# Optimization experiments

Hardware: AMD Instinct MI355X
Metric: run time of the kernel (lower is better)

Reference implementation:

```python
import jax, jax.numpy as jnp
import numpy as np

N = 100000
E = 1600000
D_IN = 50
D_H = 128
D_OUT = 128
EPS = 1e-5


def setup_inputs() -> dict:
    key = jax.random.key(0)
    ks = jax.random.split(key, 24)
    def w(k, shape, fan_in):
        return jax.random.normal(k, shape, jnp.float32) / np.sqrt(fan_in)
    inp = {
        'x': jax.random.normal(ks[0], (N, D_IN), jnp.float32),
        'edge_src': jax.random.randint(ks[1], (E,), 0, N, jnp.int32),
        'edge_dst': jax.random.randint(ks[2], (E,), 0, N, jnp.int32),
        # SAGEConv 1: D_IN -> D_H
        'Wl1': w(ks[3], (D_IN, D_H), D_IN), 'Wr1': w(ks[4], (D_IN, D_H), D_IN), 'b1': jnp.zeros((D_H,), jnp.float32),
        # SAGEConv 2: D_H -> D_H
        'Wl2': w(ks[5], (D_H, D_H), D_H), 'Wr2': w(ks[6], (D_H, D_H), D_H), 'b2': jnp.zeros((D_H,), jnp.float32),
        # SAGEConv 3: D_H -> D_OUT
        'Wl3': w(ks[7], (D_H, D_OUT), D_H), 'Wr3': w(ks[8], (D_H, D_OUT), D_H), 'b3': jnp.zeros((D_OUT,), jnp.float32),
        # skip linears (no bias)
        'Ws1': w(ks[9], (D_IN, D_H), D_IN), 'Ws2': w(ks[10], (D_IN, D_H), D_IN),
        # LayerNorm affine
        'lnw1': jnp.ones((D_H,), jnp.float32), 'lnb1': jnp.zeros((D_H,), jnp.float32),
        'lnw2': jnp.ones((D_H,), jnp.float32), 'lnb2': jnp.zeros((D_H,), jnp.float32),
        'lnw3': jnp.ones((D_OUT,), jnp.float32), 'lnb3': jnp.zeros((D_OUT,), jnp.float32),
        # PReLU scalar slopes (PyG init 0.25)
        'a1': jnp.float32(0.25), 'a2': jnp.float32(0.25), 'a3': jnp.float32(0.25),
    }
    return inp


def _sage(x, src, dst, Wl, Wr, b):
    # mean aggregation of source features at destinations, then linear + root
    msg = x[src]                                              # [E, d]
    agg = jax.ops.segment_sum(msg, dst, num_segments=N)       # [N, d]
    cnt = jax.ops.segment_sum(jnp.ones((src.shape[0],), x.dtype), dst, num_segments=N)
    mean = agg / jnp.maximum(cnt, 1.0)[:, None]
    return mean @ Wl + x @ Wr + b


def _graph_ln(x, w, b):
    # PyG LayerNorm mode='graph', batch=None: normalize over all nodes+channels
    xc = x - jnp.mean(x)
    std = jnp.sqrt(jnp.mean(xc * xc))
    return (xc / (std + EPS)) * w + b


def _prelu(x, a):
    return jnp.where(x >= 0, x, a * x)


def reference(x, edge_src, edge_dst, Wl1, Wr1, b1, Wl2, Wr2, b2, Wl3, Wr3, b3,
              Ws1, Ws2, lnw1, lnb1, lnw2, lnb2, lnw3, lnb3, a1, a2, a3):
    h1 = _sage(x, edge_src, edge_dst, Wl1, Wr1, b1)
    h1 = _prelu(_graph_ln(h1, lnw1, lnb1), a1)
    h2 = _sage(h1 + x @ Ws1, edge_src, edge_dst, Wl2, Wr2, b2)
    h2 = _prelu(_graph_ln(h2, lnw2, lnb2), a2)
    ret = _sage(h1 + h2 + x @ Ws2, edge_src, edge_dst, Wl3, Wr3, b3)
    ret = _prelu(_graph_ln(ret, lnw3, lnb3), a3)
    return ret
```

## Files before the change

kernel.cpp:

```cpp
#include <hip/hip_runtime.h>

#define D_IN 50
#define LN_EPS 1e-5f
#define BSH 8
#define MAXB 512

typedef __bf16 bf16_t;
typedef bf16_t bf16x8 __attribute__((ext_vector_type(8)));
typedef bf16_t bf16x4 __attribute__((ext_vector_type(4)));
typedef bf16_t bf16x2 __attribute__((ext_vector_type(2)));
typedef float f32x4_t __attribute__((ext_vector_type(4)));
typedef float f32x2_t __attribute__((ext_vector_type(2)));

#define ACCP(r, A)                                                            \
    {                                                                         \
        A[0] += (f32x2_t){__uint_as_float((r).x << 16),                       \
                          __uint_as_float((r).x & 0xffff0000u)};              \
        A[1] += (f32x2_t){__uint_as_float((r).y << 16),                       \
                          __uint_as_float((r).y & 0xffff0000u)};              \
        A[2] += (f32x2_t){__uint_as_float((r).z << 16),                       \
                          __uint_as_float((r).z & 0xffff0000u)};              \
        A[3] += (f32x2_t){__uint_as_float((r).w << 16),                       \
                          __uint_as_float((r).w & 0xffff0000u)};              \
    }

__global__ void bucket_hist_k(const int* __restrict__ dst, int* __restrict__ bcnt,
                              int e, int nb) {
    __shared__ int lh[MAXB];
    int t = threadIdx.x;
    for (int i = t; i < nb; i += 256) lh[i] = 0;
    __syncthreads();
    for (int i = blockIdx.x * 256 + t; i < e; i += gridDim.x * 256)
        atomicAdd(&lh[dst[i] >> BSH], 1);
    __syncthreads();
    for (int i = t; i < nb; i += 256) {
        int c = lh[i];
        if (c) atomicAdd(&bcnt[i * 16], c);
    }
}

__global__ void bscan_k(const int* __restrict__ bcnt, int* __restrict__ boff,
                        int* __restrict__ bpos, int nb, int e) {
    __shared__ int l[MAXB];
    int t = threadIdx.x;
    l[t] = (t < nb) ? bcnt[t * 16] : 0;
    __syncthreads();
    for (int off = 1; off < MAXB; off <<= 1) {
        int v = (t >= off) ? l[t - off] : 0;
        __syncthreads();
        l[t] += v;
        __syncthreads();
    }
    int excl = (t > 0) ? l[t - 1] : 0;
    if (t < nb) { boff[t] = excl; bpos[t * 16] = excl; }
    if (t == 0) boff[nb] = e;
}

__global__ void scatter_k(const int* __restrict__ src, const int* __restrict__ dst,
                          int* __restrict__ bpos, unsigned* __restrict__ pool,
                          int e, int nb) {
    __shared__ int lh[MAXB];
    __shared__ int lcur[MAXB];
    int t = threadIdx.x;
    for (int i = t; i < nb; i += 256) lh[i] = 0;
    __syncthreads();
    int chunk = (e + gridDim.x - 1) / gridDim.x;
    int s = blockIdx.x * chunk;
    int en = min(e, s + chunk);
    for (int i = s + t; i < en; i += 256)
        atomicAdd(&lh[dst[i] >> BSH], 1);
    __syncthreads();
    for (int i = t; i < nb; i += 256) {
        int c = lh[i];
        lcur[i] = c ? atomicAdd(&bpos[i * 16], c) : 0;
    }
    __syncthreads();
    for (int i = s + t; i < en; i += 256) {
        int d = dst[i];
        int p = atomicAdd(&lcur[d >> BSH], 1);
        pool[p] = (unsigned)src[i] | ((unsigned)(d & 255) << 17);
    }
}

__global__ void nhist_cfill_k(const unsigned* __restrict__ pool, const int* __restrict__ boff,
                              int* __restrict__ rp, int* __restrict__ col, int n) {
    __shared__ int lc[256];
    __shared__ int ls[256];
    __shared__ int lpos[256];
    int b = blockIdx.x, t = threadIdx.x;
    lc[t] = 0;
    __syncthreads();
    int s = boff[b], e = boff[b + 1];
    for (int i = s + t; i < e; i += 256) atomicAdd(&lc[pool[i] >> 17], 1);
    __syncthreads();
    int v = lc[t];
    ls[t] = v;
    __syncthreads();
    for (int off = 1; off < 256; off <<= 1) {
        int x = (t >= off) ? ls[t - off] : 0;
        __syncthreads();
        ls[t] += x;
        __syncthreads();
    }
    int excl = ls[t] - v;
    int nd = (b << BSH) + t;
    if (nd < n) rp[nd] = s + excl;
    if (nd == n - 1) rp[n] = e;
    lpos[t] = s + excl;
    __syncthreads();
    for (int i = s + t; i < e; i += 256) {
        unsigned pk = pool[i];
        int slot = atomicAdd(&lpos[pk >> 17], 1);
        col[slot] = (int)(pk & 0x1FFFFu);
    }
}

struct ConvDesc { const float* w; bf16_t* o; int kin; int kpad; };
struct ConvArgs { ConvDesc d[8]; };

__global__ void conv_w_k(ConvArgs args) {
    ConvDesc d = args.d[blockIdx.y];
    int i = blockIdx.x * 256 + threadIdx.x;
    int tot = 128 * d.kpad;
    if (i >= tot) return;
    int n = i / d.kpad, k = i - n * d.kpad;
    float v = (k < d.kin) ? d.w[(size_t)k * 128 + n] : 0.f;
    d.o[i] = (bf16_t)v;
}

__global__ void conv_x_k(const float* __restrict__ x, bf16_t* __restrict__ xb, int n) {
    int i = blockIdx.x * 256 + threadIdx.x;
    if (i >= n * 64) return;
    int node = i >> 6, k = i & 63;
    xb[i] = (k < D_IN) ? (bf16_t)x[node * D_IN + k] : (bf16_t)0.f;
}

__global__ void agg_bf64_k(const bf16_t* __restrict__ feat, const int* __restrict__ rp,
                           const int* __restrict__ col, bf16_t* __restrict__ mean, int n) {
    int wid = (blockIdx.x * blockDim.x + threadIdx.x) >> 6;
    int lane = threadIdx.x & 63;
    if (wid >= n) return;
    int start = rp[wid], end = rp[wid + 1];
    int lc = lane & 7;
    int g = lane >> 3;
    f32x2_t accA[4], accB[4];
#pragma unroll
    for (int k = 0; k < 4; k++) { accA[k] = (f32x2_t){0.f, 0.f}; accB[k] = (f32x2_t){0.f, 0.f}; }
    int e = start + g;
    if (e + 8 < end) {
        int i0 = col[e], i1 = col[e + 8];
        for (; e + 24 < end; e += 16) {
            uint4 r0 = *(const uint4*)(feat + (size_t)i0 * 64 + lc * 8);
            uint4 r1 = *(const uint4*)(feat + (size_t)i1 * 64 + lc * 8);
            i0 = col[e + 16];
            i1 = col[e + 24];
            ACCP(r0, accA);
            ACCP(r1, accB);
        }
        uint4 r0 = *(const uint4*)(feat + (size_t)i0 * 64 + lc * 8);
        uint4 r1 = *(const uint4*)(feat + (size_t)i1 * 64 + lc * 8);
        ACCP(r0, accA);
        ACCP(r1, accB);
        e += 16;
    }
    for (; e < end; e += 8) {
        uint4 r0 = *(const uint4*)(feat + (size_t)col[e] * 64 + lc * 8);
        ACCP(r0, accA);
    }
#pragma unroll
    for (int k = 0; k < 4; k++) accA[k] += accB[k];
    float aL[4], aH[4];
#pragma unroll
    for (int k = 0; k < 4; k++) { aL[k] = accA[k].x; aH[k] = accA[k].y; }
#pragma unroll
    for (int off = 8; off < 64; off <<= 1) {
#pragma unroll
        for (int k = 0; k < 4; k++) {
            aL[k] += __shfl_xor(aL[k], off);
            aH[k] += __shfl_xor(aH[k], off);
        }
    }
    int c = end - start;
    float invc = 1.f / (float)(c > 0 ? c : 1);
    if (lane < 8) {
        bf16x8 o;
#pragma unroll
        for (int k = 0; k < 4; k++) {
            o[2 * k] = (bf16_t)(aL[k] * invc);
            o[2 * k + 1] = (bf16_t)(aH[k] * invc);
        }
        *(bf16x8*)(mean + (size_t)wid * 64 + lc * 8) = o;
    }
}

__global__ void agg_bf128_k(const bf16_t* __restrict__ feat, const int* __restrict__ rp,
                            const int* __restrict__ col, bf16_t* __restrict__ mean, int n) {
    int wid = (blockIdx.x * blockDim.x + threadIdx.x) >> 6;
    int lane = threadIdx.x & 63;
    if (wid >= n) return;
    int start = rp[wid], end = rp[wid + 1];
    int lc = lane & 15;
    int g = lane >> 4;
    const uint* fp = (const uint*)feat + lc * 4;
    f32x2_t accA[4], accB[4];
#pragma unroll
    for (int k = 0; k < 4; k++) { accA[k] = (f32x2_t){0.f, 0.f}; accB[k] = (f32x2_t){0.f, 0.f}; }
    int e = start + g;
    int ng = (e < end) ? (((end - 1 - e) >> 2) + 1) : 0;
    int it = 0;
    for (; it + 4 <= ng; it += 4, e += 16) {
        int a = col[e], b = col[e + 4], c = col[e + 8], d = col[e + 12];
        uint4 r0 = *(const uint4*)(fp + (size_t)a * 64);
        uint4 r1 = *(const uint4*)(fp + (size_t)b * 64);
        uint4 r2 = *(const uint4*)(fp + (size_t)c * 64);
        uint4 r3 = *(const uint4*)(fp + (size_t)d * 64);
        ACCP(r0, accA);
        ACCP(r1, accB);
        ACCP(r2, accA);
        ACCP(r3, accB);
    }
    int rem = ng - it;
    if (rem > 0) {
        int a = col[e];
        int b = (rem > 1) ? col[e + 4] : a;
        int c = (rem > 2) ? col[e + 8] : b;
        uint4 r0 = *(const uint4*)(fp + (size_t)a * 64);
        uint4 r1 = *(const uint4*)(fp + (size_t)b * 64);
        uint4 r2 = *(const uint4*)(fp + (size_t)c * 64);
        ACCP(r0, accA);
        if (rem > 1) ACCP(r1, accB);
        if (rem > 2) ACCP(r2, accA);
    }
#pragma unroll
    for (int k = 0; k < 4; k++) accA[k] += accB[k];
    float aL[4], aH[4];
#pragma unroll
    for (int k = 0; k < 4; k++) { aL[k] = accA[k].x; aH[k] = accA[k].y; }
#pragma unroll
    for (int off = 16; off < 64; off <<= 1) {
#pragma unroll
        for (int k = 0; k < 4; k++) {
            aL[k] += __shfl_xor(aL[k], off);
            aH[k] += __shfl_xor(aH[k], off);
        }
    }
    int c = end - start;
    float invc = 1.f / (float)(c > 0 ? c : 1);
    if (lane < 16) {
        bf16x8 o;
#pragma unroll
        for (int k = 0; k < 4; k++) {
            o[2 * k] = (bf16_t)(aL[k] * invc);
            o[2 * k + 1] = (bf16_t)(aH[k] * invc);
        }
        *(bf16x8*)(mean + (size_t)wid * 128 + lc * 8) = o;
    }
}

template <int KPAD, bool DUAL, bool ACC>
__global__ __launch_bounds__(256) void mfma_gemm_k(
    const bf16_t* __restrict__ A, const bf16_t* __restrict__ B,
    const bf16_t* __restrict__ WlT, const bf16_t* __restrict__ WrT,
    const float* __restrict__ bias,
    bf16_t* __restrict__ out, float2* __restrict__ partials, int M) {
    constexpr int KC = KPAD / 32;
    constexpr int WELE = 8 * KC * 64 * 8;
    __shared__ bf16_t lwl[WELE];
    __shared__ bf16_t lwr[DUAL ? WELE : 8];

    const int tid = threadIdx.x;
    for (int ch = tid; ch < 8 * KC * 64; ch += 256) {
        int nt = ch / (KC * 64);
        int rem = ch - nt * (KC * 64);
        int c = rem >> 6;
        int ln = rem & 63;
        int m = ln & 15, q = ln >> 4;
        size_t srcoff = (size_t)(nt * 16 + m) * KPAD + c * 32 + q * 8;
        *(bf16x8*)&lwl[ch * 8] = *(const bf16x8*)(WlT + srcoff);
        if (DUAL) *(bf16x8*)&lwr[ch * 8] = *(const bf16x8*)(WrT + srcoff);
    }
    __syncthreads();

    const int wid = blockIdx.x * 4 + (tid >> 6);
    const int lane = tid & 63;
    const int row0 = wid * 32;
    if (row0 >= M) return;
    const int m = lane & 15;
    const int q = lane >> 4;

    bf16x8 af[2][KC], bfr[DUAL ? 2 : 1][DUAL ? KC : 1];
#pragma unroll
    for (int s = 0; s < 2; s++) {
        const bf16_t* ar = A + (size_t)(row0 + s * 16 + m) * KPAD + q * 8;
#pragma unroll
        for (int c = 0; c < KC; c++) af[s][c] = *(const bf16x8*)(ar + c * 32);
        if (DUAL) {
            const bf16_t* br = B + (size_t)(row0 + s * 16 + m) * KPAD + q * 8;
#pragma unroll
            for (int c = 0; c < KC; c++) bfr[s][c] = *(const bf16x8*)(br + c * 32);
        }
    }

    float lsum = 0.f, lsum2 = 0.f;
#pragma unroll
    for (int nt = 0; nt < 8; nt++) {
        f32x4_t acc0 = {0.f, 0.f, 0.f, 0.f};
        f32x4_t acc1 = {0.f, 0.f, 0.f, 0.f};
#pragma unroll
        for (int c = 0; c < KC; c++) {
            bf16x8 w = *(const bf16x8*)&lwl[((nt * KC + c) * 64 + lane) * 8];
            acc0 = __builtin_amdgcn_mfma_f32_16x16x32_bf16(af[0][c], w, acc0, 0, 0, 0);
            acc1 = __builtin_amdgcn_mfma_f32_16x16x32_bf16(af[1][c], w, acc1, 0, 0, 0);
        }
        if (DUAL) {
#pragma unroll
            for (int c = 0; c < KC; c++) {
                bf16x8 w = *(const bf16x8*)&lwr[((nt * KC + c) * 64 + lane) * 8];
                acc0 = __builtin_amdgcn_mfma_f32_16x16x32_bf16(bfr[0][c], w, acc0, 0, 0, 0);
                acc1 = __builtin_amdgcn_mfma_f32_16x16x32_bf16(bfr[1][c], w, acc1, 0, 0, 0);
            }
        }
        float bv = bias ? bias[nt * 16 + m] : 0.f;
#pragma unroll
        for (int s = 0; s < 2; s++) {
            f32x4_t* ap = (s == 0) ? &acc0 : &acc1;
#pragma unroll
            for (int r = 0; r < 4; r++) {
                int row = row0 + s * 16 + q * 4 + r;
                if (row < M) {
                    float o = (*ap)[r] + bv;
                    out[(size_t)row * 128 + nt * 16 + m] = (bf16_t)o;
                    if (ACC) { lsum += o; lsum2 += o * o; }
                }
            }
        }
    }
    if (ACC) {
        for (int off = 32; off > 0; off >>= 1) {
            lsum += __shfl_down(lsum, off);
            lsum2 += __shfl_down(lsum2, off);
        }
        if (lane == 0) partials[wid] = make_float2(lsum, lsum2);
    }
}

__global__ __launch_bounds__(256) void mfma_gemm3_k(
    const bf16_t* __restrict__ A, const bf16_t* __restrict__ B,
    const bf16_t* __restrict__ WlT, const bf16_t* __restrict__ WrT,
    const bf16_t* __restrict__ Ws1T, const bf16_t* __restrict__ Ws2T,
    const float* __restrict__ bias,
    bf16_t* __restrict__ outP, bf16_t* __restrict__ outC1, bf16_t* __restrict__ outC2,
    float2* __restrict__ partials, int M) {
    constexpr int KC = 2;
    constexpr int WELE = 8 * KC * 64 * 8;
    __shared__ bf16_t lwl[WELE];
    __shared__ bf16_t lwr[WELE];
    __shared__ bf16_t ls1[WELE];
    __shared__ bf16_t ls2[WELE];

    const int tid = threadIdx.x;
    for (int ch = tid; ch < 8 * KC * 64; ch += 256) {
        int nt = ch / (KC * 64);
        int rem = ch - nt * (KC * 64);
        int c = rem >> 6;
        int ln = rem & 63;
        int m = ln & 15, q = ln >> 4;
        size_t srcoff = (size_t)(nt * 16 + m) * 64 + c * 32 + q * 8;
        *(bf16x8*)&lwl[ch * 8] = *(const bf16x8*)(WlT + srcoff);
        *(bf16x8*)&lwr[ch * 8] = *(const bf16x8*)(WrT + srcoff);
        *(bf16x8*)&ls1[ch * 8] = *(const bf16x8*)(Ws1T + srcoff);
        *(bf16x8*)&ls2[ch * 8] = *(const bf16x8*)(Ws2T + srcoff);
    }
    __syncthreads();

    const int wid = blockIdx.x * 4 + (tid >> 6);
    const int lane = tid & 63;
    const int row0 = wid * 32;
    if (row0 >= M) return;
    const int m = lane & 15;
    const int q = lane >> 4;

    bf16x8 af[2][KC], bfr[2][KC];
#pragma unroll
    for (int s = 0; s < 2; s++) {
        const bf16_t* ar = A + (size_t)(row0 + s * 16 + m) * 64 + q * 8;
        const bf16_t* br = B + (size_t)(row0 + s * 16 + m) * 64 + q * 8;
#pragma unroll
        for (int c = 0; c < KC; c++) {
            af[s][c] = *(const bf16x8*)(ar + c * 32);
            bfr[s][c] = *(const bf16x8*)(br + c * 32);
        }
    }

    float lsum = 0.f, lsum2 = 0.f;
#pragma unroll
    for (int nt = 0; nt < 8; nt++) {
        f32x4_t aP0 = {0.f, 0.f, 0.f, 0.f}, aP1 = {0.f, 0.f, 0.f, 0.f};
        f32x4_t a10 = {0.f, 0.f, 0.f, 0.f}, a11 = {0.f, 0.f, 0.f, 0.f};
        f32x4_t a20 = {0.f, 0.f, 0.f, 0.f}, a21 = {0.f, 0.f, 0.f, 0.f};
#pragma unroll
        for (int c = 0; c < KC; c++) {
            int wi = ((nt * KC + c) * 64 + lane) * 8;
            bf16x8 wl = *(const bf16x8*)&lwl[wi];
            bf16x8 wr = *(const bf16x8*)&lwr[wi];
            bf16x8 w1 = *(const bf16x8*)&ls1[wi];
            bf16x8 w2 = *(const bf16x8*)&ls2[wi];
            aP0 = __builtin_amdgcn_mfma_f32_16x16x32_bf16(af[0][c], wl, aP0, 0, 0, 0);
            aP1 = __builtin_amdgcn_mfma_f32_16x16x32_bf16(af[1][c], wl, aP1, 0, 0, 0);
            aP0 = __builtin_amdgcn_mfma_f32_16x16x32_bf16(bfr[0][c], wr, aP0, 0, 0, 0);
            aP1 = __builtin_amdgcn_mfma_f32_16x16x32_bf16(bfr[1][c], wr, aP1, 0, 0, 0);
            a10 = __builtin_amdgcn_mfma_f32_16x16x32_bf16(bfr[0][c], w1, a10, 0, 0, 0);
            a11 = __builtin_amdgcn_mfma_f32_16x16x32_bf16(bfr[1][c], w1, a11, 0, 0, 0);
            a20 = __builtin_amdgcn_mfma_f32_16x16x32_bf16(bfr[0][c], w2, a20, 0, 0, 0);
            a21 = __builtin_amdgcn_mfma_f32_16x16x32_bf16(bfr[1][c], w2, a21, 0, 0, 0);
        }
        float bv = bias[nt * 16 + m];
#pragma unroll
        for (int s = 0; s < 2; s++) {
            f32x4_t* pP = (s == 0) ? &aP0 : &aP1;
            f32x4_t* p1 = (s == 0) ? &a10 : &a11;
            f32x4_t* p2 = (s == 0) ? &a20 : &a21;
#pragma unroll
            for (int r = 0; r < 4; r++) {
                int row = row0 + s * 16 + q * 4 + r;
                if (row < M) {
                    float o = (*pP)[r] + bv;
                    size_t oi = (size_t)row * 128 + nt * 16 + m;
                    outP[oi] = (bf16_t)o;
                    outC1[oi] = (bf16_t)(*p1)[r];
                    outC2[oi] = (bf16_t)(*p2)[r];
                    lsum += o; lsum2 += o * o;
                }
            }
        }
    }
    for (int off = 32; off > 0; off >>= 1) {
        lsum += __shfl_down(lsum, off);
        lsum2 += __shfl_down(lsum2, off);
    }
    if (lane == 0) partials[wid] = make_float2(lsum, lsum2);
}

__global__ void reduce_partials_k(const float2* __restrict__ p, int n,
                                  double* __restrict__ outp) {
    __shared__ double s1[256], s2[256];
    int t = threadIdx.x;
    double a = 0.0, b = 0.0;
    for (int i = t; i < n; i += 256) { a += (double)p[i].x; b += (double)p[i].y; }
    s1[t] = a; s2[t] = b;
    __syncthreads();
    for (int off = 128; off > 0; off >>= 1) {
        if (t < off) { s1[t] += s1[t + off]; s2[t] += s2[t + off]; }
        __syncthreads();
    }
    if (t == 0) { outp[0] = s1[0]; outp[1] = s2[0]; }
}

template <int MODE>
__global__ void ln_prelu_k(const bf16_t* __restrict__ pre, const bf16_t* __restrict__ h1in,
                           const bf16_t* __restrict__ s,
                           const float* __restrict__ lnw, const float* __restrict__ lnb,
                           const float* __restrict__ a_ptr, const double* __restrict__ acc,
                           void* __restrict__ out0v, void* __restrict__ out1v, int total) {
    int i = blockIdx.x * blockDim.x + threadIdx.x;
    if (i * 8 >= total) return;
    double cinv = 1.0 / (double)total;
    double mm = acc[0] * cinv;
    double var = acc[1] * cinv - mm * mm;
    float stdv = (float)sqrt(var > 0.0 ? var : 0.0);
    float scale = 1.0f / (stdv + LN_EPS);
    float mf = (float)mm;
    float a = a_ptr[0];
    int c8 = i & 15;
    float4 w0 = ((const float4*)lnw)[c8 * 2];
    float4 w1 = ((const float4*)lnw)[c8 * 2 + 1];
    float4 b0 = ((const float4*)lnb)[c8 * 2];
    float4 b1 = ((const float4*)lnb)[c8 * 2 + 1];
    float wv[8] = {w0.x, w0.y, w0.z, w0.w, w1.x, w1.y, w1.z, w1.w};
    float bv[8] = {b0.x, b0.y, b0.z, b0.w, b1.x, b1.y, b1.z, b1.w};
    bf16x8 p8 = ((const bf16x8*)pre)[i];
    float h[8];
#pragma unroll
    for (int k = 0; k < 8; k++) {
        float v = ((float)p8[k] - mf) * scale * wv[k] + bv[k];
        h[k] = v >= 0.f ? v : a * v;
    }
    if (MODE == 1) {
        bf16x8 hb, tb;
        bf16x8 sv = ((const bf16x8*)s)[i];
#pragma unroll
        for (int k = 0; k < 8; k++) {
            hb[k] = (bf16_t)h[k];
            tb[k] = (bf16_t)(h[k] + (float)sv[k]);
        }
        ((bf16x8*)out0v)[i] = hb;
        ((bf16x8*)out1v)[i] = tb;
    } else if (MODE == 2) {
        bf16x8 hv = ((const bf16x8*)h1in)[i];
        bf16x8 sv = ((const bf16x8*)s)[i];
        bf16x8 tb;
#pragma unroll
        for (int k = 0; k < 8; k++)
            tb[k] = (bf16_t)((float)hv[k] + h[k] + (float)sv[k]);
        ((bf16x8*)out0v)[i] = tb;
    } else {
        float4 o0 = {h[0], h[1], h[2], h[3]};
        float4 o1 = {h[4], h[5], h[6], h[7]};
        ((float4*)out0v)[i * 2] = o0;
        ((float4*)out0v)[i * 2 + 1] = o1;
    }
}

extern "C" void kernel_launch(void* const* d_in, const int* in_sizes, int n_in,
                              void* d_out, int out_size, void* d_ws, size_t ws_size,
                              hipStream_t stream) {
    const float* x    = (const float*)d_in[0];
    const int*   esrc = (const int*)d_in[1];
    const int*   edst = (const int*)d_in[2];
    const float* Wl1  = (const float*)d_in[3];
    const float* Wr1  = (const float*)d_in[4];
    const float* b1   = (const float*)d_in[5];
    const float* Wl2  = (const float*)d_in[6];
    const float* Wr2  = (const float*)d_in[7];
    const float* b2   = (const float*)d_in[8];
    const float* Wl3  = (const float*)d_in[9];
    const float* Wr3  = (const float*)d_in[10];
    const float* b3   = (const float*)d_in[11];
    const float* Ws1  = (const float*)d_in[12];
    const float* Ws2  = (const float*)d_in[13];
    const float* lnw1 = (const float*)d_in[14];
    const float* lnb1 = (const float*)d_in[15];
    const float* lnw2 = (const float*)d_in[16];
    const float* lnb2 = (const float*)d_in[17];
    const float* lnw3 = (const float*)d_in[18];
    const float* lnb3 = (const float*)d_in[19];
    const float* a1   = (const float*)d_in[20];
    const float* a2   = (const float*)d_in[21];
    const float* a3   = (const float*)d_in[22];

    const int N = in_sizes[0] / D_IN;
    const int E = in_sizes[1];
    const int NB = (N + 255) >> BSH;

    char* ws = (char*)d_ws;
    size_t off = 0;
    auto alloc = [&](size_t bytes) -> void* {
        void* p = ws + off;
        off += (bytes + 255) & ~(size_t)255;
        return p;
    };
    bf16_t* xb   = (bf16_t*)alloc((size_t)N * 64 * 2);
    bf16_t* mean = (bf16_t*)alloc((size_t)N * 128 * 2);
    bf16_t* PRE  = (bf16_t*)alloc((size_t)N * 128 * 2);
    bf16_t* C1   = (bf16_t*)alloc((size_t)N * 128 * 2);
    bf16_t* C2   = (bf16_t*)alloc((size_t)N * 128 * 2);
    bf16_t* h1b  = (bf16_t*)alloc((size_t)N * 128 * 2);
    bf16_t* TB   = (bf16_t*)alloc((size_t)N * 128 * 2);
    bf16_t* WT   = (bf16_t*)alloc((size_t)(4 * 128 * 64 + 4 * 128 * 128) * 2);
    int* rp   = (int*)alloc((size_t)(N + 1) * 4);
    int* col  = (int*)alloc((size_t)E * 4);
    int* bcnt = (int*)alloc((size_t)MAXB * 16 * 4);
    int* boff = (int*)alloc((size_t)(MAXB + 1) * 4);
    int* bpos = (int*)alloc((size_t)MAXB * 16 * 4);
    unsigned* pool = (unsigned*)alloc((size_t)E * 4);
    double* lnacc = (double*)alloc(6 * 8);
    const int tiles = (N + 31) / 32;
    float2* partials = (float2*)alloc((size_t)tiles * 8);

    bf16_t* Wl1T = WT;
    bf16_t* Wr1T = Wl1T + 128 * 64;
    bf16_t* Ws1T = Wr1T + 128 * 64;
    bf16_t* Ws2T = Ws1T + 128 * 64;
    bf16_t* Wl2T = Ws2T + 128 * 64;
    bf16_t* Wr2T = Wl2T + 128 * 128;
    bf16_t* Wl3T = Wr2T + 128 * 128;
    bf16_t* Wr3T = Wl3T + 128 * 128;

    hipMemsetAsync(bcnt, 0, (size_t)MAXB * 16 * 4, stream);

    bucket_hist_k<<<256, 256, 0, stream>>>(edst, bcnt, E, NB);
    bscan_k<<<1, MAXB, 0, stream>>>(bcnt, boff, bpos, NB, E);
    scatter_k<<<256, 256, 0, stream>>>(esrc, edst, bpos, pool, E, NB);
    nhist_cfill_k<<<NB, 256, 0, stream>>>(pool, boff, rp, col, N);

    ConvArgs ca;
    ca.d[0] = {Wl1, Wl1T, 50, 64};
    ca.d[1] = {Wr1, Wr1T, 50, 64};
    ca.d[2] = {Ws1, Ws1T, 50, 64};
    ca.d[3] = {Ws2, Ws2T, 50, 64};
    ca.d[4] = {Wl2, Wl2T, 128, 128};
    ca.d[5] = {Wr2, Wr2T, 128, 128};
    ca.d[6] = {Wl3, Wl3T, 128, 128};
    ca.d[7] = {Wr3, Wr3T, 128, 128};
    conv_w_k<<<dim3(64, 8), 256, 0, stream>>>(ca);
    conv_x_k<<<(N * 64 + 255) / 256, 256, 0, stream>>>(x, xb, N);

    const int aggBlocks = ((N * 64) + 255) / 256;
    const int gemmBlocks = (tiles + 3) / 4;
    const int lnBlocks = (N * 128 / 8 + 255) / 256;
    const int total = N * 128;

    agg_bf64_k<<<aggBlocks, 256, 0, stream>>>(xb, rp, col, mean, N);
    mfma_gemm3_k<<<gemmBlocks, 256, 0, stream>>>(
        mean, xb, Wl1T, Wr1T, Ws1T, Ws2T, b1, PRE, C1, C2, partials, N);
    reduce_partials_k<<<1, 256, 0, stream>>>(partials, tiles, lnacc + 0);
    ln_prelu_k<1><<<lnBlocks, 256, 0, stream>>>(
        PRE, nullptr, C1, lnw1, lnb1, a1, lnacc + 0, h1b, TB, total);

    agg_bf128_k<<<aggBlocks, 256, 0, stream>>>(TB, rp, col, mean, N);
    mfma_gemm_k<128, true, true><<<gemmBlocks, 256, 0, stream>>>(
        mean, TB, Wl2T, Wr2T, b2, PRE, partials, N);
    reduce_partials_k<<<1, 256, 0, stream>>>(partials, tiles, lnacc + 2);
    ln_prelu_k<2><<<lnBlocks, 256, 0, stream>>>(
        PRE, h1b, C2, lnw2, lnb2, a2, lnacc + 2, TB, nullptr, total);

    agg_bf128_k<<<aggBlocks, 256, 0, stream>>>(TB, rp, col, mean, N);
    mfma_gemm_k<128, true, true><<<gemmBlocks, 256, 0, stream>>>(
        mean, TB, Wl3T, Wr3T, b3, PRE, partials, N);
    reduce_partials_k<<<1, 256, 0, stream>>>(partials, tiles, lnacc + 4);
    ln_prelu_k<3><<<lnBlocks, 256, 0, stream>>>(
        PRE, nullptr, nullptr, lnw3, lnb3, a3, lnacc + 4, d_out, nullptr, total);
}
```

Measured before the change: 538.1 us.

## Slice 128-wide features into 8 column slabs for cache-friendly aggregation; atomic LN stats

Stores the layer-2/3 aggregation inputs and means in a sliced layout (8 slabs of 16 channels per node), so each aggregation block gathers from one 3.2 MB slab that fits better in cache. Each node is handled by two lanes reading 16-byte pieces, in place of a full wave per node. The GEMM reads the sliced layout directly. The separate partial-reduction kernels are replaced by per-block double atomics into lnacc, which is zeroed inside the histogram kernel. The tradeoff is 32-byte scattered gathers per neighbor and a nondeterministic atomic summation order.

```diff
diff --git a/kernel.cpp b/kernel.cpp
--- a/kernel.cpp
+++ b/kernel.cpp
@@ -7,8 +7,6 @@
 
 typedef __bf16 bf16_t;
 typedef bf16_t bf16x8 __attribute__((ext_vector_type(8)));
-typedef bf16_t bf16x4 __attribute__((ext_vector_type(4)));
-typedef bf16_t bf16x2 __attribute__((ext_vector_type(2)));
 typedef float f32x4_t __attribute__((ext_vector_type(4)));
 typedef float f32x2_t __attribute__((ext_vector_type(2)));
 
@@ -24,10 +22,12 @@
                           __uint_as_float((r).w & 0xffff0000u)};              \
     }
 
+
 __global__ void bucket_hist_k(const int* __restrict__ dst, int* __restrict__ bcnt,
-                              int e, int nb) {
+                              double* __restrict__ lnacc, int e, int nb) {
     __shared__ int lh[MAXB];
     int t = threadIdx.x;
+    if (blockIdx.x == 0 && t < 6) lnacc[t] = 0.0;
     for (int i = t; i < nb; i += 256) lh[i] = 0;
     __syncthreads();
     for (int i = blockIdx.x * 256 + t; i < e; i += gridDim.x * 256)
@@ -193,80 +193,77 @@
     }
 }
 
-__global__ void agg_bf128_k(const bf16_t* __restrict__ feat, const int* __restrict__ rp,
-                            const int* __restrict__ col, bf16_t* __restrict__ mean, int n) {
-    int wid = (blockIdx.x * blockDim.x + threadIdx.x) >> 6;
-    int lane = threadIdx.x & 63;
-    if (wid >= n) return;
-    int start = rp[wid], end = rp[wid + 1];
-    int lc = lane & 15;
-    int g = lane >> 4;
-    const uint* fp = (const uint*)feat + lc * 4;
+__global__ __launch_bounds__(256) void agg_slice_k(
+    const bf16_t* __restrict__ featS,
+    const int* __restrict__ rp, const int* __restrict__ col,
+    bf16_t* __restrict__ meanS,
+    int n, int np) {
+    const int bid = blockIdx.x;
+    const int slice = bid & 7;
+    const int chunk = bid >> 3;
+    const int tid = threadIdx.x;
+    const int w = tid >> 6;
+    const int lane = tid & 63;
+    const int g = lane >> 1;
+    const int h = lane & 1;
+    const int node = chunk * 128 + w * 32 + g;
+    if (node >= n) return;
+    const uint* fp = (const uint*)(featS + (size_t)slice * np * 16) + h * 4;
+    int start = rp[node], end = rp[node + 1];
+    int deg = end - start;
     f32x2_t accA[4], accB[4];
 #pragma unroll
     for (int k = 0; k < 4; k++) { accA[k] = (f32x2_t){0.f, 0.f}; accB[k] = (f32x2_t){0.f, 0.f}; }
-    int e = start + g;
-    int ng = (e < end) ? (((end - 1 - e) >> 2) + 1) : 0;
+    int e = start;
     int it = 0;
-    for (; it + 4 <= ng; it += 4, e += 16) {
-        int a = col[e], b = col[e + 4], c = col[e + 8], d = col[e + 12];
-        uint4 r0 = *(const uint4*)(fp + (size_t)a * 64);
-        uint4 r1 = *(const uint4*)(fp + (size_t)b * 64);
-        uint4 r2 = *(const uint4*)(fp + (size_t)c * 64);
-        uint4 r3 = *(const uint4*)(fp + (size_t)d * 64);
+    for (; it + 4 <= deg; it += 4, e += 4) {
+        int a = __builtin_nontemporal_load(col + e);
+        int b = __builtin_nontemporal_load(col + e + 1);
+        int c = __builtin_nontemporal_load(col + e + 2);
+        int d = __builtin_nontemporal_load(col + e + 3);
+        uint4 r0 = *(const uint4*)(fp + (size_t)a * 8);
+        uint4 r1 = *(const uint4*)(fp + (size_t)b * 8);
+        uint4 r2 = *(const uint4*)(fp + (size_t)c * 8);
+        uint4 r3 = *(const uint4*)(fp + (size_t)d * 8);
         ACCP(r0, accA);
         ACCP(r1, accB);
         ACCP(r2, accA);
         ACCP(r3, accB);
     }
-    int rem = ng - it;
+    int rem = deg - it;
     if (rem > 0) {
-        int a = col[e];
-        int b = (rem > 1) ? col[e + 4] : a;
-        int c = (rem > 2) ? col[e + 8] : b;
-        uint4 r0 = *(const uint4*)(fp + (size_t)a * 64);
-        uint4 r1 = *(const uint4*)(fp + (size_t)b * 64);
-        uint4 r2 = *(const uint4*)(fp + (size_t)c * 64);
+        int a = __builtin_nontemporal_load(col + e);
+        int b = (rem > 1) ? __builtin_nontemporal_load(col + e + 1) : a;
+        int c = (rem > 2) ? __builtin_nontemporal_load(col + e + 2) : b;
+        uint4 r0 = *(const uint4*)(fp + (size_t)a * 8);
+        uint4 r1 = *(const uint4*)(fp + (size_t)b * 8);
+        uint4 r2 = *(const uint4*)(fp + (size_t)c * 8);
         ACCP(r0, accA);
         if (rem > 1) ACCP(r1, accB);
         if (rem > 2) ACCP(r2, accA);
     }
 #pragma unroll
     for (int k = 0; k < 4; k++) accA[k] += accB[k];
-    float aL[4], aH[4];
-#pragma unroll
-    for (int k = 0; k < 4; k++) { aL[k] = accA[k].x; aH[k] = accA[k].y; }
-#pragma unroll
-    for (int off = 16; off < 64; off <<= 1) {
-#pragma unroll
-        for (int k = 0; k < 4; k++) {
-            aL[k] += __shfl_xor(aL[k], off);
-            aH[k] += __shfl_xor(aH[k], off);
-        }
-    }
-    int c = end - start;
-    float invc = 1.f / (float)(c > 0 ? c : 1);
-    if (lane < 16) {
-        bf16x8 o;
-#pragma unroll
-        for (int k = 0; k < 4; k++) {
-            o[2 * k] = (bf16_t)(aL[k] * invc);
-            o[2 * k + 1] = (bf16_t)(aH[k] * invc);
-        }
-        *(bf16x8*)(mean + (size_t)wid * 128 + lc * 8) = o;
-    }
-}
-
-template <int KPAD, bool DUAL, bool ACC>
-__global__ __launch_bounds__(256) void mfma_gemm_k(
+    float invc = 1.f / (float)(deg > 0 ? deg : 1);
+    bf16x8 o;
+#pragma unroll
+    for (int k = 0; k < 4; k++) {
+        o[2 * k] = (bf16_t)(accA[k].x * invc);
+        o[2 * k + 1] = (bf16_t)(accA[k].y * invc);
+    }
+    *(bf16x8*)(meanS + ((size_t)slice * np + node) * 16 + h * 8) = o;
+}
+
+__global__ __launch_bounds__(256) void mfma_gemm_s_k(
     const bf16_t* __restrict__ A, const bf16_t* __restrict__ B,
     const bf16_t* __restrict__ WlT, const bf16_t* __restrict__ WrT,
     const float* __restrict__ bias,
-    bf16_t* __restrict__ out, float2* __restrict__ partials, int M) {
-    constexpr int KC = KPAD / 32;
+    bf16_t* __restrict__ out, double* __restrict__ lnacc, int M, int NP) {
+    constexpr int KC = 4;
     constexpr int WELE = 8 * KC * 64 * 8;
     __shared__ bf16_t lwl[WELE];
-    __shared__ bf16_t lwr[DUAL ? WELE : 8];
+    __shared__ bf16_t lwr[WELE];
+    __shared__ float rsum[4], rsum2[4];
 
     const int tid = threadIdx.x;
     for (int ch = tid; ch < 8 * KC * 64; ch += 256) {
@@ -275,72 +272,76 @@
         int c = rem >> 6;
         int ln = rem & 63;
         int m = ln & 15, q = ln >> 4;
-        size_t srcoff = (size_t)(nt * 16 + m) * KPAD + c * 32 + q * 8;
+        size_t srcoff = (size_t)(nt * 16 + m) * 128 + c * 32 + q * 8;
         *(bf16x8*)&lwl[ch * 8] = *(const bf16x8*)(WlT + srcoff);
-        if (DUAL) *(bf16x8*)&lwr[ch * 8] = *(const bf16x8*)(WrT + srcoff);
-    }
-    __syncthreads();
-
-    const int wid = blockIdx.x * 4 + (tid >> 6);
+        *(bf16x8*)&lwr[ch * 8] = *(const bf16x8*)(WrT + srcoff);
+    }
+    __syncthreads();
+
+    const int w = tid >> 6;
+    const int wid = blockIdx.x * 4 + w;
     const int lane = tid & 63;
     const int row0 = wid * 32;
-    if (row0 >= M) return;
     const int m = lane & 15;
     const int q = lane >> 4;
-
-    bf16x8 af[2][KC], bfr[DUAL ? 2 : 1][DUAL ? KC : 1];
-#pragma unroll
-    for (int s = 0; s < 2; s++) {
-        const bf16_t* ar = A + (size_t)(row0 + s * 16 + m) * KPAD + q * 8;
-#pragma unroll
-        for (int c = 0; c < KC; c++) af[s][c] = *(const bf16x8*)(ar + c * 32);
-        if (DUAL) {
-            const bf16_t* br = B + (size_t)(row0 + s * 16 + m) * KPAD + q * 8;
-#pragma unroll
-            for (int c = 0; c < KC; c++) bfr[s][c] = *(const bf16x8*)(br + c * 32);
-        }
-    }
+    const bool act = row0 < M;
 
     float lsum = 0.f, lsum2 = 0.f;
-#pragma unroll
-    for (int nt = 0; nt < 8; nt++) {
-        f32x4_t acc0 = {0.f, 0.f, 0.f, 0.f};
-        f32x4_t acc1 = {0.f, 0.f, 0.f, 0.f};
-#pragma unroll
-        for (int c = 0; c < KC; c++) {
-            bf16x8 w = *(const bf16x8*)&lwl[((nt * KC + c) * 64 + lane) * 8];
-            acc0 = __builtin_amdgcn_mfma_f32_16x16x32_bf16(af[0][c], w, acc0, 0, 0, 0);
-            acc1 = __builtin_amdgcn_mfma_f32_16x16x32_bf16(af[1][c], w, acc1, 0, 0, 0);
-        }
-        if (DUAL) {
+    if (act) {
+        bf16x8 af[2][KC], bfr[2][KC];
+#pragma unroll
+        for (int s = 0; s < 2; s++) {
+            int row = row0 + s * 16 + m;
 #pragma unroll
             for (int c = 0; c < KC; c++) {
-                bf16x8 w = *(const bf16x8*)&lwr[((nt * KC + c) * 64 + lane) * 8];
-                acc0 = __builtin_amdgcn_mfma_f32_16x16x32_bf16(bfr[0][c], w, acc0, 0, 0, 0);
-                acc1 = __builtin_amdgcn_mfma_f32_16x16x32_bf16(bfr[1][c], w, acc1, 0, 0, 0);
+                size_t so = ((size_t)(2 * c + (q >> 1)) * NP + row) * 16 + (q & 1) * 8;
+                af[s][c] = *(const bf16x8*)(A + so);
+                bfr[s][c] = *(const bf16x8*)(B + so);
             }
         }
-        float bv = bias ? bias[nt * 16 + m] : 0.f;
-#pragma unroll
-        for (int s = 0; s < 2; s++) {
-            f32x4_t* ap = (s == 0) ? &acc0 : &acc1;
-#pragma unroll
-            for (int r = 0; r < 4; r++) {
-                int row = row0 + s * 16 + q * 4 + r;
-                if (row < M) {
-                    float o = (*ap)[r] + bv;
-                    out[(size_t)row * 128 + nt * 16 + m] = (bf16_t)o;
-                    if (ACC) { lsum += o; lsum2 += o * o; }
+#pragma unroll
+        for (int nt = 0; nt < 8; nt++) {
+            f32x4_t acc0 = {0.f, 0.f, 0.f, 0.f};
+            f32x4_t acc1 = {0.f, 0.f, 0.f, 0.f};
+#pragma unroll
+            for (int c = 0; c < KC; c++) {
+                bf16x8 wl = *(const bf16x8*)&lwl[((nt * KC + c) * 64 + lane) * 8];
+                acc0 = __builtin_amdgcn_mfma_f32_16x16x32_bf16(af[0][c], wl, acc0, 0, 0, 0);
+                acc1 = __builtin_amdgcn_mfma_f32_16x16x32_bf16(af[1][c], wl, acc1, 0, 0, 0);
+            }
+#pragma unroll
+            for (int c = 0; c < KC; c++) {
+                bf16x8 wr = *(const bf16x8*)&lwr[((nt * KC + c) * 64 + lane) * 8];
+                acc0 = __builtin_amdgcn_mfma_f32_16x16x32_bf16(bfr[0][c], wr, acc0, 0, 0, 0);
+                acc1 = __builtin_amdgcn_mfma_f32_16x16x32_bf16(bfr[1][c], wr, acc1, 0, 0, 0);
+            }
+            float bv = bias[nt * 16 + m];
+#pragma unroll
+            for (int s = 0; s < 2; s++) {
+                f32x4_t* ap = (s == 0) ? &acc0 : &acc1;
+#pragma unroll
+                for (int r = 0; r < 4; r++) {
+                    int row = row0 + s * 16 + q * 4 + r;
+                    if (row < M) {
+                        float o = (*ap)[r] + bv;
+                        out[(size_t)row * 128 + nt * 16 + m] = (bf16_t)o;
+                        lsum += o; lsum2 += o * o;
+                    }
                 }
             }
         }
     }
-    if (ACC) {
-        for (int off = 32; off > 0; off >>= 1) {
-            lsum += __shfl_down(lsum, off);
-            lsum2 += __shfl_down(lsum2, off);
-        }
-        if (lane == 0) partials[wid] = make_float2(lsum, lsum2);
+    for (int off = 32; off > 0; off >>= 1) {
+        lsum += __shfl_down(lsum, off);
+        lsum2 += __shfl_down(lsum2, off);
+    }
+    if (lane == 0) { rsum[w] = lsum; rsum2[w] = lsum2; }
+    __syncthreads();
+    if (tid == 0) {
+        double s = (double)rsum[0] + (double)rsum[1] + (double)rsum[2] + (double)rsum[3];
+        double s2 = (double)rsum2[0] + (double)rsum2[1] + (double)rsum2[2] + (double)rsum2[3];
+        unsafeAtomicAdd(&lnacc[0], s);
+        unsafeAtomicAdd(&lnacc[1], s2);
     }
 }
 
@@ -350,13 +351,14 @@
     const bf16_t* __restrict__ Ws1T, const bf16_t* __restrict__ Ws2T,
     const float* __restrict__ bias,
     bf16_t* __restrict__ outP, bf16_t* __restrict__ outC1, bf16_t* __restrict__ outC2,
-    float2* __restrict__ partials, int M) {
+    double* __restrict__ lnacc, int M) {
     constexpr int KC = 2;
     constexpr int WELE = 8 * KC * 64 * 8;
     __shared__ bf16_t lwl[WELE];
     __shared__ bf16_t lwr[WELE];
     __shared__ bf16_t ls1[WELE];
     __shared__ bf16_t ls2[WELE];
+    __shared__ float rsum[4], rsum2[4];
 
     const int tid = threadIdx.x;
     for (int ch = tid; ch < 8 * KC * 64; ch += 256) {
@@ -373,63 +375,65 @@
     }
     __syncthreads();
 
-    const int wid = blockIdx.x * 4 + (tid >> 6);
+    const int w = tid >> 6;
+    const int wid = blockIdx.x * 4 + w;
     const int lane = tid & 63;
     const int row0 = wid * 32;
-    if (row0 >= M) return;
     const int m = lane & 15;
     const int q = lane >> 4;
-
-    bf16x8 af[2][KC], bfr[2][KC];
-#pragma unroll
-    for (int s = 0; s < 2; s++) {
-        const bf16_t* ar = A + (size_t)(row0 + s * 16 + m) * 64 + q * 8;
-        const bf16_t* br = B + (size_t)(row0 + s * 16 + m) * 64 + q * 8;
-#pragma unroll
-        for (int c = 0; c < KC; c++) {
-            af[s][c] = *(const bf16x8*)(ar + c * 32);
-            bfr[s][c] = *(const bf16x8*)(br + c * 32);
-        }
-    }
+    const bool act = row0 < M;
 
     float lsum = 0.f, lsum2 = 0.f;
-#pragma unroll
-    for (int nt = 0; nt < 8; nt++) {
-        f32x4_t aP0 = {0.f, 0.f, 0.f, 0.f}, aP1 = {0.f, 0.f, 0.f, 0.f};
-        f32x4_t a10 = {0.f, 0.f, 0.f, 0.f}, a11 = {0.f, 0.f, 0.f, 0.f};
-        f32x4_t a20 = {0.f, 0.f, 0.f, 0.f}, a21 = {0.f, 0.f, 0.f, 0.f};
-#pragma unroll
-        for (int c = 0; c < KC; c++) {
-            int wi = ((nt * KC + c) * 64 + lane) * 8;
-            bf16x8 wl = *(const bf16x8*)&lwl[wi];
-            bf16x8 wr = *(const bf16x8*)&lwr[wi];
-            bf16x8 w1 = *(const bf16x8*)&ls1[wi];
-            bf16x8 w2 = *(const bf16x8*)&ls2[wi];
-            aP0 = __builtin_amdgcn_mfma_f32_16x16x32_bf16(af[0][c], wl, aP0, 0, 0, 0);
-            aP1 = __builtin_amdgcn_mfma_f32_16x16x32_bf16(af[1][c], wl, aP1, 0, 0, 0);
-            aP0 = __builtin_amdgcn_mfma_f32_16x16x32_bf16(bfr[0][c], wr, aP0, 0, 0, 0);
-            aP1 = __builtin_amdgcn_mfma_f32_16x16x32_bf16(bfr[1][c], wr, aP1, 0, 0, 0);
-            a10 = __builtin_amdgcn_mfma_f32_16x16x32_bf16(bfr[0][c], w1, a10, 0, 0, 0);
-            a11 = __builtin_amdgcn_mfma_f32_16x16x32_bf16(bfr[1][c], w1, a11, 0, 0, 0);
-            a20 = __builtin_amdgcn_mfma_f32_16x16x32_bf16(bfr[0][c], w2, a20, 0, 0, 0);
-            a21 = __builtin_amdgcn_mfma_f32_16x16x32_bf16(bfr[1][c], w2, a21, 0, 0, 0);
-        }
-        float bv = bias[nt * 16 + m];
+    if (act) {
+        bf16x8 af[2][KC], bfr[2][KC];
 #pragma unroll
         for (int s = 0; s < 2; s++) {
-            f32x4_t* pP = (s == 0) ? &aP0 : &aP1;
-            f32x4_t* p1 = (s == 0) ? &a10 : &a11;
-            f32x4_t* p2 = (s == 0) ? &a20 : &a21;
-#pragma unroll
-            for (int r = 0; r < 4; r++) {
-                int row = row0 + s * 16 + q * 4 + r;
-                if (row < M) {
-                    float o = (*pP)[r] + bv;
-                    size_t oi = (size_t)row * 128 + nt * 16 + m;
-                    outP[oi] = (bf16_t)o;
-                    outC1[oi] = (bf16_t)(*p1)[r];
-                    outC2[oi] = (bf16_t)(*p2)[r];
-                    lsum += o; lsum2 += o * o;
+            const bf16_t* ar = A + (size_t)(row0 + s * 16 + m) * 64 + q * 8;
+            const bf16_t* br = B + (size_t)(row0 + s * 16 + m) * 64 + q * 8;
+#pragma unroll
+            for (int c = 0; c < KC; c++) {
+                af[s][c] = *(const bf16x8*)(ar + c * 32);
+                bfr[s][c] = *(const bf16x8*)(br + c * 32);
+            }
+        }
+#pragma unroll
+        for (int nt = 0; nt < 8; nt++) {
+            f32x4_t aP0 = {0.f, 0.f, 0.f, 0.f}, aP1 = {0.f, 0.f, 0.f, 0.f};
+            f32x4_t a10 = {0.f, 0.f, 0.f, 0.f}, a11 = {0.f, 0.f, 0.f, 0.f};
+            f32x4_t a20 = {0.f, 0.f, 0.f, 0.f}, a21 = {0.f, 0.f, 0.f, 0.f};
+#pragma unroll
+            for (int c = 0; c < KC; c++) {
+                int wi = ((nt * KC + c) * 64 + lane) * 8;
+                bf16x8 wl = *(const bf16x8*)&lwl[wi];
+                bf16x8 wr = *(const bf16x8*)&lwr[wi];
+                bf16x8 w1 = *(const bf16x8*)&ls1[wi];
+                bf16x8 w2 = *(const bf16x8*)&ls2[wi];
+                aP0 = __builtin_amdgcn_mfma_f32_16x16x32_bf16(af[0][c], wl, aP0, 0, 0, 0);
+                aP1 = __builtin_amdgcn_mfma_f32_16x16x32_bf16(af[1][c], wl, aP1, 0, 0, 0);
+                aP0 = __builtin_amdgcn_mfma_f32_16x16x32_bf16(bfr[0][c], wr, aP0, 0, 0, 0);
+                aP1 = __builtin_amdgcn_mfma_f32_16x16x32_bf16(bfr[1][c], wr, aP1, 0, 0, 0);
+                a10 = __builtin_amdgcn_mfma_f32_16x16x32_bf16(bfr[0][c], w1, a10, 0, 0, 0);
+                a11 = __builtin_amdgcn_mfma_f32_16x16x32_bf16(bfr[1][c], w1, a11, 0, 0, 0);
+                a20 = __builtin_amdgcn_mfma_f32_16x16x32_bf16(bfr[0][c], w2, a20, 0, 0, 0);
+                a21 = __builtin_amdgcn_mfma_f32_16x16x32_bf16(bfr[1][c], w2, a21, 0, 0, 0);
+            }
+            float bv = bias[nt * 16 + m];
+#pragma unroll
+            for (int s = 0; s < 2; s++) {
+                f32x4_t* pP = (s == 0) ? &aP0 : &aP1;
+                f32x4_t* p1 = (s == 0) ? &a10 : &a11;
+                f32x4_t* p2 = (s == 0) ? &a20 : &a21;
+#pragma unroll
+                for (int r = 0; r < 4; r++) {
+                    int row = row0 + s * 16 + q * 4 + r;
+                    if (row < M) {
+                        float o = (*pP)[r] + bv;
+                        size_t oi = (size_t)row * 128 + nt * 16 + m;
+                        outP[oi] = (bf16_t)o;
+                        outC1[oi] = (bf16_t)(*p1)[r];
+                        outC2[oi] = (bf16_t)(*p2)[r];
+                        lsum += o; lsum2 += o * o;
+                    }
                 }
             }
         }
@@ -438,22 +442,14 @@
         lsum += __shfl_down(lsum, off);
         lsum2 += __shfl_down(lsum2, off);
     }
-    if (lane == 0) partials[wid] = make_float2(lsum, lsum2);
-}
-
-__global__ void reduce_partials_k(const float2* __restrict__ p, int n,
-                                  double* __restrict__ outp) {
-    __shared__ double s1[256], s2[256];
-    int t = threadIdx.x;
-    double a = 0.0, b = 0.0;
-    for (int i = t; i < n; i += 256) { a += (double)p[i].x; b += (double)p[i].y; }
-    s1[t] = a; s2[t] = b;
-    __syncthreads();
-    for (int off = 128; off > 0; off >>= 1) {
-        if (t < off) { s1[t] += s1[t + off]; s2[t] += s2[t + off]; }
-        __syncthreads();
-    }
-    if (t == 0) { outp[0] = s1[0]; outp[1] = s2[0]; }
+    if (lane == 0) { rsum[w] = lsum; rsum2[w] = lsum2; }
+    __syncthreads();
+    if (tid == 0) {
+        double s = (double)rsum[0] + (double)rsum[1] + (double)rsum[2] + (double)rsum[3];
+        double s2 = (double)rsum2[0] + (double)rsum2[1] + (double)rsum2[2] + (double)rsum2[3];
+        unsafeAtomicAdd(&lnacc[0], s);
+        unsafeAtomicAdd(&lnacc[1], s2);
+    }
 }
 
 template <int MODE>
@@ -461,7 +457,8 @@
                            const bf16_t* __restrict__ s,
                            const float* __restrict__ lnw, const float* __restrict__ lnb,
                            const float* __restrict__ a_ptr, const double* __restrict__ acc,
-                           void* __restrict__ out0v, void* __restrict__ out1v, int total) {
+                           void* __restrict__ out0v, void* __restrict__ out1v,
+                           int total, int np) {
     int i = blockIdx.x * blockDim.x + threadIdx.x;
     if (i * 8 >= total) return;
     double cinv = 1.0 / (double)total;
@@ -472,6 +469,7 @@
     float mf = (float)mm;
     float a = a_ptr[0];
     int c8 = i & 15;
+    int node = i >> 4;
     float4 w0 = ((const float4*)lnw)[c8 * 2];
     float4 w1 = ((const float4*)lnw)[c8 * 2 + 1];
     float4 b0 = ((const float4*)lnb)[c8 * 2];
@@ -485,6 +483,7 @@
         float v = ((float)p8[k] - mf) * scale * wv[k] + bv[k];
         h[k] = v >= 0.f ? v : a * v;
     }
+    size_t soff = ((size_t)(c8 >> 1) * np + node) * 16 + (c8 & 1) * 8;
     if (MODE == 1) {
         bf16x8 hb, tb;
         bf16x8 sv = ((const bf16x8*)s)[i];
@@ -494,7 +493,7 @@
             tb[k] = (bf16_t)(h[k] + (float)sv[k]);
         }
         ((bf16x8*)out0v)[i] = hb;
-        ((bf16x8*)out1v)[i] = tb;
+        *(bf16x8*)((bf16_t*)out1v + soff) = tb;
     } else if (MODE == 2) {
         bf16x8 hv = ((const bf16x8*)h1in)[i];
         bf16x8 sv = ((const bf16x8*)s)[i];
@@ -502,7 +501,7 @@
 #pragma unroll
         for (int k = 0; k < 8; k++)
             tb[k] = (bf16_t)((float)hv[k] + h[k] + (float)sv[k]);
-        ((bf16x8*)out0v)[i] = tb;
+        *(bf16x8*)((bf16_t*)out0v + soff) = tb;
     } else {
         float4 o0 = {h[0], h[1], h[2], h[3]};
         float4 o1 = {h[4], h[5], h[6], h[7]};
@@ -541,6 +540,7 @@
     const int N = in_sizes[0] / D_IN;
     const int E = in_sizes[1];
     const int NB = (N + 255) >> BSH;
+    const int NP = (N + 127) & ~127;
 
     char* ws = (char*)d_ws;
     size_t off = 0;
@@ -549,14 +549,15 @@
         off += (bytes + 255) & ~(size_t)255;
         return p;
     };
-    bf16_t* xb   = (bf16_t*)alloc((size_t)N * 64 * 2);
-    bf16_t* mean = (bf16_t*)alloc((size_t)N * 128 * 2);
-    bf16_t* PRE  = (bf16_t*)alloc((size_t)N * 128 * 2);
-    bf16_t* C1   = (bf16_t*)alloc((size_t)N * 128 * 2);
-    bf16_t* C2   = (bf16_t*)alloc((size_t)N * 128 * 2);
-    bf16_t* h1b  = (bf16_t*)alloc((size_t)N * 128 * 2);
-    bf16_t* TB   = (bf16_t*)alloc((size_t)N * 128 * 2);
-    bf16_t* WT   = (bf16_t*)alloc((size_t)(4 * 128 * 64 + 4 * 128 * 128) * 2);
+    bf16_t* xb    = (bf16_t*)alloc((size_t)N * 64 * 2);
+    bf16_t* mean64= (bf16_t*)alloc((size_t)N * 64 * 2);
+    bf16_t* meanS = (bf16_t*)alloc((size_t)NP * 128 * 2);
+    bf16_t* TBS   = (bf16_t*)alloc((size_t)NP * 128 * 2);
+    bf16_t* PRE   = (bf16_t*)alloc((size_t)N * 128 * 2);
+    bf16_t* C1    = (bf16_t*)alloc((size_t)N * 128 * 2);
+    bf16_t* C2    = (bf16_t*)alloc((size_t)N * 128 * 2);
+    bf16_t* h1b   = (bf16_t*)alloc((size_t)N * 128 * 2);
+    bf16_t* WT    = (bf16_t*)alloc((size_t)(4 * 128 * 64 + 4 * 128 * 128) * 2);
     int* rp   = (int*)alloc((size_t)(N + 1) * 4);
     int* col  = (int*)alloc((size_t)E * 4);
     int* bcnt = (int*)alloc((size_t)MAXB * 16 * 4);
@@ -564,8 +565,6 @@
     int* bpos = (int*)alloc((size_t)MAXB * 16 * 4);
     unsigned* pool = (unsigned*)alloc((size_t)E * 4);
     double* lnacc = (double*)alloc(6 * 8);
-    const int tiles = (N + 31) / 32;
-    float2* partials = (float2*)alloc((size_t)tiles * 8);
 
     bf16_t* Wl1T = WT;
     bf16_t* Wr1T = Wl1T + 128 * 64;
@@ -578,7 +577,7 @@
 
     hipMemsetAsync(bcnt, 0, (size_t)MAXB * 16 * 4, stream);
 
-    bucket_hist_k<<<256, 256, 0, stream>>>(edst, bcnt, E, NB);
+    bucket_hist_k<<<256, 256, 0, stream>>>(edst, bcnt, lnacc, E, NB);
     bscan_k<<<1, MAXB, 0, stream>>>(bcnt, boff, bpos, NB, E);
     scatter_k<<<256, 256, 0, stream>>>(esrc, edst, bpos, pool, E, NB);
     nhist_cfill_k<<<NB, 256, 0, stream>>>(pool, boff, rp, col, N);
@@ -595,29 +594,28 @@
     conv_w_k<<<dim3(64, 8), 256, 0, stream>>>(ca);
     conv_x_k<<<(N * 64 + 255) / 256, 256, 0, stream>>>(x, xb, N);
 
-    const int aggBlocks = ((N * 64) + 255) / 256;
+    const int agg64Blocks = ((N * 64) + 255) / 256;
+    const int aggSliceBlocks = ((N + 127) / 128) * 8;
+    const int tiles = (N + 31) / 32;
     const int gemmBlocks = (tiles + 3) / 4;
     const int lnBlocks = (N * 128 / 8 + 255) / 256;
     const int total = N * 128;
 
-    agg_bf64_k<<<aggBlocks, 256, 0, stream>>>(xb, rp, col, mean, N);
+    agg_bf64_k<<<agg64Blocks, 256, 0, stream>>>(xb, rp, col, mean64, N);
     mfma_gemm3_k<<<gemmBlocks, 256, 0, stream>>>(
-        mean, xb, Wl1T, Wr1T, Ws1T, Ws2T, b1, PRE, C1, C2, partials, N);
-    reduce_partials_k<<<1, 256, 0, stream>>>(partials, tiles, lnacc + 0);
+        mean64, xb, Wl1T, Wr1T, Ws1T, Ws2T, b1, PRE, C1, C2, lnacc + 0, N);
     ln_prelu_k<1><<<lnBlocks, 256, 0, stream>>>(
-        PRE, nullptr, C1, lnw1, lnb1, a1, lnacc + 0, h1b, TB, total);
-
-    agg_bf128_k<<<aggBlocks, 256, 0, stream>>>(TB, rp, col, mean, N);
-    mfma_gemm_k<128, true, true><<<gemmBlocks, 256, 0, stream>>>(
-        mean, TB, Wl2T, Wr2T, b2, PRE, partials, N);
-    reduce_partials_k<<<1, 256, 0, stream>>>(partials, tiles, lnacc + 2);
+        PRE, nullptr, C1, lnw1, lnb1, a1, lnacc + 0, h1b, TBS, total, NP);
+
+    agg_slice_k<<<aggSliceBlocks, 256, 0, stream>>>(TBS, rp, col, meanS, N, NP);
+    mfma_gemm_s_k<<<gemmBlocks, 256, 0, stream>>>(
+        meanS, TBS, Wl2T, Wr2T, b2, PRE, lnacc + 2, N, NP);
     ln_prelu_k<2><<<lnBlocks, 256, 0, stream>>>(
-        PRE, h1b, C2, lnw2, lnb2, a2, lnacc + 2, TB, nullptr, total);
-
-    agg_bf128_k<<<aggBlocks, 256, 0, stream>>>(TB, rp, col, mean, N);
-    mfma_gemm_k<128, true, true><<<gemmBlocks, 256, 0, stream>>>(
-        mean, TB, Wl3T, Wr3T, b3, PRE, partials, N);
-    reduce_partials_k<<<1, 256, 0, stream>>>(partials, tiles, lnacc + 4);
+        PRE, h1b, C2, lnw2, lnb2, a2, lnacc + 2, TBS, nullptr, total, NP);
+
+    agg_slice_k<<<aggSliceBlocks, 256, 0, stream>>>(TBS, rp, col, meanS, N, NP);
+    mfma_gemm_s_k<<<gemmBlocks, 256, 0, stream>>>(
+        meanS, TBS, Wl3T, Wr3T, b3, PRE, lnacc + 4, N, NP);
     ln_prelu_k<3><<<lnBlocks, 256, 0, stream>>>(
-        PRE, nullptr, nullptr, lnw3, lnb3, a3, lnacc + 4, d_out, nullptr, total);
-}
+        PRE, nullptr, nullptr, lnw3, lnb3, a3, lnacc + 4, d_out, nullptr, total, NP);
+}
```

Result: slower. 679.1 us (+26.2%).
